# Optimization experiments

Measured on AMD Instinct MI355X. Metric: run time of the kernel, lower is better.

Reference implementation:

```python
import jax, jax.numpy as jnp
import numpy as np

N = 4096
IN_F = 256
OUT_F = 32
H = 8
NEG_SLOPE = 0.2
EDGE_P = 0.004  # avg degree ~16


def setup_inputs() -> dict:
    key = jax.random.key(0)
    k1, k2, k3, k4, k5 = jax.random.split(key, 5)
    x = jax.random.normal(k1, (N, IN_F), dtype=jnp.float32)
    adj = jax.random.bernoulli(k2, EDGE_P, (N, N))  # bool sparse-ish adjacency
    # xavier-uniform-ish scales
    w_scale = np.sqrt(6.0 / (IN_F + OUT_F))
    a_scale = np.sqrt(6.0 / (OUT_F + 1))
    W = jax.random.uniform(k3, (H, IN_F, OUT_F), jnp.float32, -w_scale, w_scale)
    a_src = jax.random.uniform(k4, (H, OUT_F), jnp.float32, -a_scale, a_scale)
    a_dst = jax.random.uniform(k5, (H, OUT_F), jnp.float32, -a_scale, a_scale)
    bias = jnp.zeros((H * OUT_F,), dtype=jnp.float32)
    return {"x": x, "adj": adj, "W": W, "a_src": a_src, "a_dst": a_dst, "bias": bias}


def reference(x, adj, W, a_src, a_dst, bias):
    n = x.shape[0]
    # adjacency mask with self-loops, (N, N)
    mask = adj | jnp.eye(n, dtype=bool)
    # Wh: (H, N, OUT_F)
    Wh = jnp.einsum('hif,ni->hnf', W, x)
    # per-node attention logits, (H, N)
    e_src = jnp.einsum('hnf,hf->hn', Wh, a_src)
    e_dst = jnp.einsum('hnf,hf->hn', Wh, a_dst)
    # additive scores, (H, N, N): row i attends over columns j
    e = e_src[:, :, None] + e_dst[:, None, :]
    e = jnp.where(e >= 0, e, NEG_SLOPE * e)  # LeakyReLU
    e = jnp.where(mask[None], e, -jnp.inf)
    alpha = jax.nn.softmax(e, axis=-1)
    # dropout p=0.6 is a no-op in eval mode
    out = jnp.einsum('hnm,hmf->hnf', alpha, Wh)
    # concat heads: (N, H*OUT_F)
    out = jnp.transpose(out, (1, 0, 2)).reshape(n, -1)
    return out + bias
```

## Files before the change

kernel.cpp:

```cpp
#include <hip/hip_runtime.h>
#include <hip/hip_bf16.h>
#include <stdint.h>

#define N_NODES 4096
#define IN_F 256
#define OUT_F 32
#define H 8
#define HF 256
#define NPB 16
#define XPAD 20
#define MAXK 128

typedef __hip_bfloat16 bf16;
__device__ __forceinline__ float b2f(bf16 v) { return __bfloat162float(v); }

__device__ __forceinline__ int detect_f32m(const void* xv, int t) {
    uint16_t u = ((const uint16_t*)xv)[t & 63];
    bf16 v = *(bf16*)&u;
    float f = b2f(v);
    int wild = !(fabsf(f) < 100.0f);
    unsigned long long ball = __ballot(wild);
    return __popcll(ball) > 4;
}

__global__ __launch_bounds__(256) void wh_kernel(
    const void* __restrict__ xv, const void* __restrict__ Wv,
    const void* __restrict__ asv, const void* __restrict__ adv,
    const uint32_t* __restrict__ adj, int* __restrict__ modes,
    float* __restrict__ Wh, float* __restrict__ esrc, float* __restrict__ edst)
{
    const int t = threadIdx.x;
    const int f32m = detect_f32m(xv, t);

    if (blockIdx.x == 256) {
        __shared__ int s[4];
        if (t < 4) s[t] = 0;
        __syncthreads();
        int E = 0, F = 0, G = 0;
        for (int i = t; i < 16384; i += 256) {
            uint32_t w = adj[i];
            if ((w >> 8) != 0) E++;
            uint32_t lo = w & 0xFFFFu, hi = w >> 16;
            if (lo == 0x3F80u || hi == 0x3F80u) F++;
            if (lo != 0) G++;
        }
        if (E) atomicAdd(&s[1], E);
        if (F) atomicAdd(&s[2], F);
        if (G) atomicAdd(&s[3], G);
        __syncthreads();
        if (t == 0) {
            int amode;
            if (s[1] == 0)               amode = 0;
            else if (s[2] > 0 && !s[3])  amode = 0;
            else if (s[2] > 0)           amode = 1;
            else                         amode = 2;
            modes[0] = f32m | (amode << 1);
        }
        return;
    }

    __shared__ float xl[IN_F][XPAD];
    const int n0 = blockIdx.x * NPB;

    if (f32m) {
        const float* x = (const float*)xv + (size_t)n0 * IN_F;
        #pragma unroll
        for (int r = 0; r < NPB; ++r) xl[t][r] = x[(size_t)r * IN_F + t];
    } else {
        const bf16* x = (const bf16*)xv + (size_t)n0 * IN_F;
        #pragma unroll
        for (int r = 0; r < NPB; ++r) xl[t][r] = b2f(x[(size_t)r * IN_F + t]);
    }
    __syncthreads();

    const int rg = t >> 6;
    const int cg = t & 63;
    const int h  = cg >> 3;
    const int f0 = (cg & 7) * 4;

    float acc[4][4];
    #pragma unroll
    for (int r = 0; r < 4; ++r)
        #pragma unroll
        for (int j = 0; j < 4; ++j) acc[r][j] = 0.f;

    if (f32m) {
        const float* Wp = (const float*)Wv + (size_t)h * IN_F * OUT_F + f0;
        #pragma unroll 4
        for (int i = 0; i < IN_F; ++i) {
            const float4 w4 = *(const float4*)&Wp[(size_t)i * OUT_F];
            const float4 x4 = *(const float4*)&xl[i][rg * 4];
            const float xs[4] = {x4.x, x4.y, x4.z, x4.w};
            #pragma unroll
            for (int r = 0; r < 4; ++r) {
                acc[r][0] += xs[r] * w4.x;
                acc[r][1] += xs[r] * w4.y;
                acc[r][2] += xs[r] * w4.z;
                acc[r][3] += xs[r] * w4.w;
            }
        }
    } else {
        const bf16* Wp = (const bf16*)Wv + (size_t)h * IN_F * OUT_F + f0;
        #pragma unroll 4
        for (int i = 0; i < IN_F; ++i) {
            const ushort4 wu = *(const ushort4*)&Wp[(size_t)i * OUT_F];
            float w0 = b2f(*(bf16*)&wu.x), w1 = b2f(*(bf16*)&wu.y);
            float w2 = b2f(*(bf16*)&wu.z), w3 = b2f(*(bf16*)&wu.w);
            const float4 x4 = *(const float4*)&xl[i][rg * 4];
            const float xs[4] = {x4.x, x4.y, x4.z, x4.w};
            #pragma unroll
            for (int r = 0; r < 4; ++r) {
                acc[r][0] += xs[r] * w0;
                acc[r][1] += xs[r] * w1;
                acc[r][2] += xs[r] * w2;
                acc[r][3] += xs[r] * w3;
            }
        }
    }

    float as0, as1, as2, as3, ad0, ad1, ad2, ad3;
    if (f32m) {
        const float4 a4 = *(const float4*)&((const float*)asv)[h * OUT_F + f0];
        const float4 b4 = *(const float4*)&((const float*)adv)[h * OUT_F + f0];
        as0 = a4.x; as1 = a4.y; as2 = a4.z; as3 = a4.w;
        ad0 = b4.x; ad1 = b4.y; ad2 = b4.z; ad3 = b4.w;
    } else {
        const ushort4 a4 = *(const ushort4*)&((const bf16*)asv)[h * OUT_F + f0];
        const ushort4 b4 = *(const ushort4*)&((const bf16*)adv)[h * OUT_F + f0];
        as0 = b2f(*(bf16*)&a4.x); as1 = b2f(*(bf16*)&a4.y);
        as2 = b2f(*(bf16*)&a4.z); as3 = b2f(*(bf16*)&a4.w);
        ad0 = b2f(*(bf16*)&b4.x); ad1 = b2f(*(bf16*)&b4.y);
        ad2 = b2f(*(bf16*)&b4.z); ad3 = b2f(*(bf16*)&b4.w);
    }

    #pragma unroll
    for (int r = 0; r < 4; ++r) {
        const int n = n0 + rg * 4 + r;
        *(float4*)&Wh[(size_t)n * HF + cg * 4] =
            make_float4(acc[r][0], acc[r][1], acc[r][2], acc[r][3]);
        float vs = acc[r][0] * as0 + acc[r][1] * as1 + acc[r][2] * as2 + acc[r][3] * as3;
        float vd = acc[r][0] * ad0 + acc[r][1] * ad1 + acc[r][2] * ad2 + acc[r][3] * ad3;
        vs += __shfl_down(vs, 4, 8); vs += __shfl_down(vs, 2, 8); vs += __shfl_down(vs, 1, 8);
        vd += __shfl_down(vd, 4, 8); vd += __shfl_down(vd, 2, 8); vd += __shfl_down(vd, 1, 8);
        if ((cg & 7) == 0) {
            esrc[(size_t)n * H + h] = vs;
            edst[(size_t)n * H + h] = vd;
        }
    }
}

__global__ __launch_bounds__(256) void gat_kernel(
    const void* __restrict__ adjv, const float* __restrict__ Wh,
    const float* __restrict__ esrc, const float* __restrict__ edst,
    const void* __restrict__ biasv, const int* __restrict__ modes,
    void* __restrict__ outv)
{
    __shared__ int   nbr[MAXK];
    __shared__ float sc[MAXK * H];
    __shared__ float inv_s[H];
    __shared__ int   cnt;

    const int i = blockIdx.x, t = threadIdx.x;
    if (t == 0) cnt = 0;
    __syncthreads();

    const int m = modes[0];
    const int amode = m >> 1;
    auto push = [&](int j) { int p = atomicAdd(&cnt, 1); if (p < MAXK) nbr[p] = j; };

    if (amode == 0) {
        const int4* row = (const int4*)((const uint32_t*)adjv + (size_t)i * N_NODES);
        for (int c = t; c < N_NODES / 4; c += 256) {
            int4 v = row[c]; int j0 = c * 4;
            if (v.x != 0 && j0     != i) push(j0);
            if (v.y != 0 && j0 + 1 != i) push(j0 + 1);
            if (v.z != 0 && j0 + 2 != i) push(j0 + 2);
            if (v.w != 0 && j0 + 3 != i) push(j0 + 3);
        }
    } else if (amode == 1) {
        const int4* row = (const int4*)((const uint16_t*)adjv + (size_t)i * N_NODES);
        for (int c = t; c < N_NODES / 8; c += 256) {
            int4 v = row[c]; int j0 = c * 8;
            uint32_t w[4] = {(uint32_t)v.x, (uint32_t)v.y, (uint32_t)v.z, (uint32_t)v.w};
            #pragma unroll
            for (int q = 0; q < 4; ++q) {
                int b0 = j0 + 2 * q;
                if ((w[q] & 0xFFFFu) && b0     != i) push(b0);
                if ((w[q] >> 16)     && b0 + 1 != i) push(b0 + 1);
            }
        }
    } else {
        const int4* row = (const int4*)((const uint8_t*)adjv + (size_t)i * N_NODES);
        for (int c = t; c < N_NODES / 16; c += 256) {
            int4 v = row[c]; int j0 = c * 16;
            uint32_t w[4] = {(uint32_t)v.x, (uint32_t)v.y, (uint32_t)v.z, (uint32_t)v.w};
            #pragma unroll
            for (int q = 0; q < 4; ++q) {
                uint32_t u = w[q]; int b0 = j0 + 4 * q;
                if ((u & 0x000000FFu) && b0     != i) push(b0);
                if ((u & 0x0000FF00u) && b0 + 1 != i) push(b0 + 1);
                if ((u & 0x00FF0000u) && b0 + 2 != i) push(b0 + 2);
                if ((u & 0xFF000000u) && b0 + 3 != i) push(b0 + 3);
            }
        }
    }
    if (t == 0) push(i);
    __syncthreads();
    const int K = cnt < MAXK ? cnt : MAXK;

    const float* esrc_i = esrc + (size_t)i * H;
    for (int idx = t; idx < K * H; idx += 256) {
        int k = idx >> 3, h = idx & 7;
        float s = esrc_i[h] + edst[(size_t)nbr[k] * H + h];
        sc[idx] = s >= 0.f ? s : 0.2f * s;
    }
    __syncthreads();

    if (t < H) {
        float mx = -1e30f;
        for (int k = 0; k < K; ++k) mx = fmaxf(mx, sc[k * H + t]);
        float sum = 0.f;
        for (int k = 0; k < K; ++k) {
            float e = __expf(sc[k * H + t] - mx);
            sc[k * H + t] = e;
            sum += e;
        }
        inv_s[t] = 1.f / sum;
    }
    __syncthreads();

    const int h = t >> 5;
    float acc = 0.f;
    #pragma unroll 4
    for (int k = 0; k < K; ++k)
        acc += sc[k * H + h] * Wh[(size_t)nbr[k] * HF + t];

    const int f32m = m & 1;
    float bias = f32m ? ((const float*)biasv)[t] : b2f(((const bf16*)biasv)[t]);
    float o = acc * inv_s[h] + bias;
    if (f32m) ((float*)outv)[(size_t)i * HF + t] = o;
    else      ((bf16*)outv)[(size_t)i * HF + t] = __float2bfloat16(o);
}

extern "C" void kernel_launch(void* const* d_in, const int* in_sizes, int n_in,
                              void* d_out, int out_size, void* d_ws, size_t ws_size,
                              hipStream_t stream) {
    const void* x     = d_in[0];
    const void* adj   = d_in[1];
    const void* W     = d_in[2];
    const void* a_src = d_in[3];
    const void* a_dst = d_in[4];
    const void* bias  = d_in[5];

    int*   modes = (int*)d_ws;
    float* Wh    = (float*)((char*)d_ws + 256);
    float* esrc  = Wh + (size_t)N_NODES * HF;
    float* edst  = esrc + (size_t)N_NODES * H;

    wh_kernel<<<N_NODES / NPB + 1, 256, 0, stream>>>(
        x, W, a_src, a_dst, (const uint32_t*)adj, modes, Wh, esrc, edst);
    gat_kernel<<<N_NODES, 256, 0, stream>>>(adj, Wh, esrc, edst, bias, modes, d_out);
}
```

Measured before the change: 137.6 us.

## Build neighbor lists concurrently with Wh projection in a fused first kernel

Moves the adjacency scan that builds per-row neighbor lists out of the attention kernel and into extra blocks of the first kernel, so it runs alongside the Wh GEMM blocks. Each build block scans 8 rows, redoes the adjacency dtype detection locally, and writes compact neighbor indices and counts to workspace. The attention kernel then only reads the precomputed lists and re-detects the input dtype itself. This hides the dense adjacency read behind the projection work, at the cost of an extra global round trip for neighbor lists and redundant dtype detection in every build block.

After: 148.0 us. 7.6% more time.

```diff
diff --git a/kernel.cpp b/kernel.cpp
--- a/kernel.cpp
+++ b/kernel.cpp
@@ -10,6 +10,8 @@
 #define NPB 16
 #define XPAD 20
 #define MAXK 128
+#define BUILD_ROWS 8
+#define NBUILD (N_NODES / BUILD_ROWS)
 
 typedef __hip_bfloat16 bf16;
 __device__ __forceinline__ float b2f(bf16 v) { return __bfloat162float(v); }
@@ -19,57 +21,116 @@
     bf16 v = *(bf16*)&u;
     float f = b2f(v);
     int wild = !(fabsf(f) < 100.0f);
-    unsigned long long ball = __ballot(wild);
-    return __popcll(ball) > 4;
-}
-
-__global__ __launch_bounds__(256) void wh_kernel(
+    return __popcll(__ballot(wild)) > 4;
+}
+
+union SmemU {
+    float xl[IN_F][XPAD];
+    struct {
+        int nbr[MAXK];
+        int cnt;
+        int s[3];
+    } b;
+};
+
+__global__ __launch_bounds__(256) void fused_kernel(
     const void* __restrict__ xv, const void* __restrict__ Wv,
     const void* __restrict__ asv, const void* __restrict__ adv,
-    const uint32_t* __restrict__ adj, int* __restrict__ modes,
-    float* __restrict__ Wh, float* __restrict__ esrc, float* __restrict__ edst)
+    const uint32_t* __restrict__ adj,
+    float* __restrict__ Wh, float* __restrict__ esrc, float* __restrict__ edst,
+    int* __restrict__ nbrs, int* __restrict__ cnts)
 {
+    __shared__ SmemU sm;
     const int t = threadIdx.x;
-    const int f32m = detect_f32m(xv, t);
-
-    if (blockIdx.x == 256) {
-        __shared__ int s[4];
-        if (t < 4) s[t] = 0;
+
+    if (blockIdx.x >= 256) {
+        const int bb = blockIdx.x - 256;
+        if (t < 3) sm.b.s[t] = 0;
+        if (t == 0) sm.b.cnt = 0;
         __syncthreads();
         int E = 0, F = 0, G = 0;
-        for (int i = t; i < 16384; i += 256) {
-            uint32_t w = adj[i];
-            if ((w >> 8) != 0) E++;
+        for (int i2 = t; i2 < 8192; i2 += 256) {
+            uint32_t w = adj[i2];
+            if (w >> 8) E++;
             uint32_t lo = w & 0xFFFFu, hi = w >> 16;
             if (lo == 0x3F80u || hi == 0x3F80u) F++;
-            if (lo != 0) G++;
-        }
-        if (E) atomicAdd(&s[1], E);
-        if (F) atomicAdd(&s[2], F);
-        if (G) atomicAdd(&s[3], G);
+            if (lo) G++;
+        }
+        if (E) atomicAdd(&sm.b.s[0], E);
+        if (F) atomicAdd(&sm.b.s[1], F);
+        if (G) atomicAdd(&sm.b.s[2], G);
         __syncthreads();
-        if (t == 0) {
-            int amode;
-            if (s[1] == 0)               amode = 0;
-            else if (s[2] > 0 && !s[3])  amode = 0;
-            else if (s[2] > 0)           amode = 1;
-            else                         amode = 2;
-            modes[0] = f32m | (amode << 1);
+        int amode;
+        {
+            int Eb = sm.b.s[0], Fb = sm.b.s[1], Gb = sm.b.s[2];
+            if (Eb == 0)                amode = 0;
+            else if (Fb > 0 && Gb == 0) amode = 0;
+            else if (Fb > 0)            amode = 1;
+            else                        amode = 2;
+        }
+        auto push = [&](int j) { int p = atomicAdd(&sm.b.cnt, 1); if (p < MAXK) sm.b.nbr[p] = j; };
+
+        for (int rr = 0; rr < BUILD_ROWS; ++rr) {
+            const int i = bb * BUILD_ROWS + rr;
+            if (amode == 0) {
+                const int4* row = (const int4*)(adj + (size_t)i * N_NODES);
+                for (int c = t; c < N_NODES / 4; c += 256) {
+                    int4 v = row[c]; int j0 = c * 4;
+                    if (v.x != 0 && j0     != i) push(j0);
+                    if (v.y != 0 && j0 + 1 != i) push(j0 + 1);
+                    if (v.z != 0 && j0 + 2 != i) push(j0 + 2);
+                    if (v.w != 0 && j0 + 3 != i) push(j0 + 3);
+                }
+            } else if (amode == 1) {
+                const int4* row = (const int4*)((const uint16_t*)adj + (size_t)i * N_NODES);
+                for (int c = t; c < N_NODES / 8; c += 256) {
+                    int4 v = row[c]; int j0 = c * 8;
+                    uint32_t w[4] = {(uint32_t)v.x, (uint32_t)v.y, (uint32_t)v.z, (uint32_t)v.w};
+                    #pragma unroll
+                    for (int q = 0; q < 4; ++q) {
+                        int b0 = j0 + 2 * q;
+                        if ((w[q] & 0xFFFFu) && b0     != i) push(b0);
+                        if ((w[q] >> 16)     && b0 + 1 != i) push(b0 + 1);
+                    }
+                }
+            } else {
+                const int4* row = (const int4*)((const uint8_t*)adj + (size_t)i * N_NODES);
+                for (int c = t; c < N_NODES / 16; c += 256) {
+                    int4 v = row[c]; int j0 = c * 16;
+                    uint32_t w[4] = {(uint32_t)v.x, (uint32_t)v.y, (uint32_t)v.z, (uint32_t)v.w};
+                    #pragma unroll
+                    for (int q = 0; q < 4; ++q) {
+                        uint32_t u = w[q]; int b0 = j0 + 4 * q;
+                        if ((u & 0x000000FFu) && b0     != i) push(b0);
+                        if ((u & 0x0000FF00u) && b0 + 1 != i) push(b0 + 1);
+                        if ((u & 0x00FF0000u) && b0 + 2 != i) push(b0 + 2);
+                        if ((u & 0xFF000000u) && b0 + 3 != i) push(b0 + 3);
+                    }
+                }
+            }
+            if (t == 0) push(i);
+            __syncthreads();
+            const int K = sm.b.cnt < MAXK ? sm.b.cnt : MAXK;
+            for (int p = t; p < K; p += 256) nbrs[(size_t)i * MAXK + p] = sm.b.nbr[p];
+            if (t == 0) cnts[i] = K;
+            __syncthreads();
+            if (t == 0) sm.b.cnt = 0;
+            __syncthreads();
         }
         return;
     }
 
-    __shared__ float xl[IN_F][XPAD];
+    const int f32m = detect_f32m(xv, t);
     const int n0 = blockIdx.x * NPB;
 
     if (f32m) {
         const float* x = (const float*)xv + (size_t)n0 * IN_F;
         #pragma unroll
-        for (int r = 0; r < NPB; ++r) xl[t][r] = x[(size_t)r * IN_F + t];
+        for (int r = 0; r < NPB; ++r) sm.xl[t][r] = x[(size_t)r * IN_F + t];
     } else {
         const bf16* x = (const bf16*)xv + (size_t)n0 * IN_F;
         #pragma unroll
-        for (int r = 0; r < NPB; ++r) xl[t][r] = b2f(x[(size_t)r * IN_F + t]);
+        for (int r = 0; r < NPB; ++r) sm.xl[t][r] = b2f(x[(size_t)r * IN_F + t]);
     }
     __syncthreads();
 
@@ -89,7 +150,7 @@
         #pragma unroll 4
         for (int i = 0; i < IN_F; ++i) {
             const float4 w4 = *(const float4*)&Wp[(size_t)i * OUT_F];
-            const float4 x4 = *(const float4*)&xl[i][rg * 4];
+            const float4 x4 = *(const float4*)&sm.xl[i][rg * 4];
             const float xs[4] = {x4.x, x4.y, x4.z, x4.w};
             #pragma unroll
             for (int r = 0; r < 4; ++r) {
@@ -106,7 +167,7 @@
             const ushort4 wu = *(const ushort4*)&Wp[(size_t)i * OUT_F];
             float w0 = b2f(*(bf16*)&wu.x), w1 = b2f(*(bf16*)&wu.y);
             float w2 = b2f(*(bf16*)&wu.z), w3 = b2f(*(bf16*)&wu.w);
-            const float4 x4 = *(const float4*)&xl[i][rg * 4];
+            const float4 x4 = *(const float4*)&sm.xl[i][rg * 4];
             const float xs[4] = {x4.x, x4.y, x4.z, x4.w};
             #pragma unroll
             for (int r = 0; r < 4; ++r) {
@@ -149,64 +210,21 @@
     }
 }
 
-__global__ __launch_bounds__(256) void gat_kernel(
-    const void* __restrict__ adjv, const float* __restrict__ Wh,
-    const float* __restrict__ esrc, const float* __restrict__ edst,
-    const void* __restrict__ biasv, const int* __restrict__ modes,
-    void* __restrict__ outv)
+__global__ __launch_bounds__(256) void gat2_kernel(
+    const float* __restrict__ Wh, const float* __restrict__ esrc,
+    const float* __restrict__ edst, const int* __restrict__ nbrs,
+    const int* __restrict__ cnts, const void* __restrict__ xv,
+    const void* __restrict__ biasv, void* __restrict__ outv)
 {
     __shared__ int   nbr[MAXK];
     __shared__ float sc[MAXK * H];
     __shared__ float inv_s[H];
-    __shared__ int   cnt;
 
     const int i = blockIdx.x, t = threadIdx.x;
-    if (t == 0) cnt = 0;
-    __syncthreads();
-
-    const int m = modes[0];
-    const int amode = m >> 1;
-    auto push = [&](int j) { int p = atomicAdd(&cnt, 1); if (p < MAXK) nbr[p] = j; };
-
-    if (amode == 0) {
-        const int4* row = (const int4*)((const uint32_t*)adjv + (size_t)i * N_NODES);
-        for (int c = t; c < N_NODES / 4; c += 256) {
-            int4 v = row[c]; int j0 = c * 4;
-            if (v.x != 0 && j0     != i) push(j0);
-            if (v.y != 0 && j0 + 1 != i) push(j0 + 1);
-            if (v.z != 0 && j0 + 2 != i) push(j0 + 2);
-            if (v.w != 0 && j0 + 3 != i) push(j0 + 3);
-        }
-    } else if (amode == 1) {
-        const int4* row = (const int4*)((const uint16_t*)adjv + (size_t)i * N_NODES);
-        for (int c = t; c < N_NODES / 8; c += 256) {
-            int4 v = row[c]; int j0 = c * 8;
-            uint32_t w[4] = {(uint32_t)v.x, (uint32_t)v.y, (uint32_t)v.z, (uint32_t)v.w};
-            #pragma unroll
-            for (int q = 0; q < 4; ++q) {
-                int b0 = j0 + 2 * q;
-                if ((w[q] & 0xFFFFu) && b0     != i) push(b0);
-                if ((w[q] >> 16)     && b0 + 1 != i) push(b0 + 1);
-            }
-        }
-    } else {
-        const int4* row = (const int4*)((const uint8_t*)adjv + (size_t)i * N_NODES);
-        for (int c = t; c < N_NODES / 16; c += 256) {
-            int4 v = row[c]; int j0 = c * 16;
-            uint32_t w[4] = {(uint32_t)v.x, (uint32_t)v.y, (uint32_t)v.z, (uint32_t)v.w};
-            #pragma unroll
-            for (int q = 0; q < 4; ++q) {
-                uint32_t u = w[q]; int b0 = j0 + 4 * q;
-                if ((u & 0x000000FFu) && b0     != i) push(b0);
-                if ((u & 0x0000FF00u) && b0 + 1 != i) push(b0 + 1);
-                if ((u & 0x00FF0000u) && b0 + 2 != i) push(b0 + 2);
-                if ((u & 0xFF000000u) && b0 + 3 != i) push(b0 + 3);
-            }
-        }
-    }
-    if (t == 0) push(i);
-    __syncthreads();
-    const int K = cnt < MAXK ? cnt : MAXK;
+    const int f32m = detect_f32m(xv, t);
+    const int K = min(cnts[i], MAXK);
+    for (int p = t; p < K; p += 256) nbr[p] = nbrs[(size_t)i * MAXK + p];
+    __syncthreads();
 
     const float* esrc_i = esrc + (size_t)i * H;
     for (int idx = t; idx < K * H; idx += 256) {
@@ -235,7 +253,6 @@
     for (int k = 0; k < K; ++k)
         acc += sc[k * H + h] * Wh[(size_t)nbr[k] * HF + t];
 
-    const int f32m = m & 1;
     float bias = f32m ? ((const float*)biasv)[t] : b2f(((const bf16*)biasv)[t]);
     float o = acc * inv_s[h] + bias;
     if (f32m) ((float*)outv)[(size_t)i * HF + t] = o;
@@ -252,12 +269,14 @@
     const void* a_dst = d_in[4];
     const void* bias  = d_in[5];
 
-    int*   modes = (int*)d_ws;
-    float* Wh    = (float*)((char*)d_ws + 256);
-    float* esrc  = Wh + (size_t)N_NODES * HF;
-    float* edst  = esrc + (size_t)N_NODES * H;
-
-    wh_kernel<<<N_NODES / NPB + 1, 256, 0, stream>>>(
-        x, W, a_src, a_dst, (const uint32_t*)adj, modes, Wh, esrc, edst);
-    gat_kernel<<<N_NODES, 256, 0, stream>>>(adj, Wh, esrc, edst, bias, modes, d_out);
-}
+    float* Wh   = (float*)((char*)d_ws + 256);
+    float* esrc = Wh + (size_t)N_NODES * HF;
+    float* edst = esrc + (size_t)N_NODES * H;
+    int*   cnts = (int*)(edst + (size_t)N_NODES * H);
+    int*   nbrs = cnts + N_NODES;
+
+    fused_kernel<<<256 + NBUILD, 256, 0, stream>>>(
+        x, W, a_src, a_dst, (const uint32_t*)adj, Wh, esrc, edst, nbrs, cnts);
+    gat2_kernel<<<N_NODES, 256, 0, stream>>>(
+        Wh, esrc, edst, nbrs, cnts, x, bias, d_out);
+}
```
